# Kernel optimization log

Measured on AMD Instinct MI355X. Metric: run time of the kernel, lower is better.

The kernel has to match this reference:

```python
import jax, jax.numpy as jnp
import numpy as np

B, C, L = 8, 1024, 1024
H = 16
D = C // H  # 64 samples per head
GROUPS = 32  # GroupNorm32: channels > 64 -> 32 groups
EPS = 1e-5


def setup_inputs() -> dict:
    key = jax.random.key(0)
    ks = jax.random.split(key, 5)
    x = jax.random.normal(ks[0], (B, C, L), dtype=jnp.float32)
    gn_weight = jnp.ones((C,), jnp.float32)
    gn_bias = jnp.zeros((C,), jnp.float32)
    qkv_w = jax.random.normal(ks[1], (3 * C, C), jnp.float32) * 0.02
    qkv_b = jax.random.normal(ks[2], (3 * C,), jnp.float32) * 0.02
    out_w = jax.random.normal(ks[3], (C, C), jnp.float32) * 0.02
    out_b = jax.random.normal(ks[4], (C,), jnp.float32) * 0.02
    return {"x": x, "gn_weight": gn_weight, "gn_bias": gn_bias,
            "qkv_w": qkv_w, "qkv_b": qkv_b, "out_w": out_w, "out_b": out_b,
            "qk_bias": 0}


def _group_norm(x, w, b):
    # x: [B, C, L]; normalize over (C//GROUPS, L) per group, in float32
    xg = x.astype(jnp.float32).reshape(B, GROUPS, -1)
    mu = xg.mean(axis=-1, keepdims=True)
    var = xg.var(axis=-1, keepdims=True)
    xn = ((xg - mu) * jax.lax.rsqrt(var + EPS)).reshape(B, C, L)
    return (xn * w[None, :, None] + b[None, :, None]).astype(x.dtype)


def reference(x, gn_weight, gn_bias, qkv_w, qkv_b, out_w, out_b, qk_bias):
    scale = 1.0 / np.sqrt(D).astype(np.float32)
    xn = _group_norm(x, gn_weight, gn_bias)
    # 1x1 conv == pointwise matmul over channels
    qkv = jnp.einsum('oc,bcl->bol', qkv_w, xn) + qkv_b[None, :, None]  # [B,3C,L]
    # reshape (B, H, 3D, L) and split exactly as torch .split(D, dim=2)
    qkv = qkv.reshape(B, H, 3 * D, L)
    q, k, v = qkv[:, :, :D], qkv[:, :, D:2 * D], qkv[:, :, 2 * D:]
    q = jnp.swapaxes(q, -1, -2) * scale  # [B,H,L,D]
    k = k * scale                        # [B,H,D,L]
    v = jnp.swapaxes(v, -1, -2)          # [B,H,L,D]
    score = jnp.einsum('bhld,bhdm->bhlm', q, k) + qk_bias  # [B,H,L,L]
    weights = jax.nn.softmax(score.astype(jnp.float32), axis=-1)
    ctx = jnp.einsum('bhlm,bhmd->bhld', weights, v)  # [B,H,L,D]
    ctx = jnp.swapaxes(ctx, -1, -2).reshape(B, C, L)
    h = jnp.einsum('oc,bcl->bol', out_w, ctx) + out_b[None, :, None]
    return xn + h  # residual uses the normalized x, as in the source
```

## Files before the change

kernel.cpp:

```cpp
#include <hip/hip_runtime.h>

using bf16x8 = __attribute__((ext_vector_type(8))) __bf16;
using f32x4  = __attribute__((ext_vector_type(4))) float;
using f32x16 = __attribute__((ext_vector_type(16))) float;
typedef __attribute__((ext_vector_type(2))) unsigned u32x2;
typedef __attribute__((ext_vector_type(4))) unsigned u32x4;

#define DEV __device__ __forceinline__

DEV unsigned short f2bf(float f){
  unsigned u = __builtin_bit_cast(unsigned, f);
  u += 0x7fffu + ((u >> 16) & 1u);
  return (unsigned short)(u >> 16);
}

DEV void load_lds16(const void* g, void* l){
  __builtin_amdgcn_global_load_lds((const __attribute__((address_space(1))) unsigned*)g,
                                   (__attribute__((address_space(3))) unsigned*)l, 16, 0, 0);
}

DEV f32x4 mfma16(bf16x8 a, bf16x8 b, f32x4 c){
  return __builtin_amdgcn_mfma_f32_16x16x32_bf16(a, b, c, 0, 0, 0);
}

DEV f32x16 mfma32(bf16x8 a, bf16x8 b, f32x16 c){
  return __builtin_amdgcn_mfma_f32_32x32x16_bf16(a, b, c, 0, 0, 0);
}

DEV float exp2_hw(float x){
  float r;
  asm("v_exp_f32 %0, %1" : "=v"(r) : "v"(x));
  return r;
}

DEV unsigned cvtpk_bf16(float a, float b){
  unsigned r;
  asm("v_cvt_pk_bf16_f32 %0, %1, %2" : "=v"(r) : "v"(a), "v"(b));
  return r;
}

DEV void permswap(unsigned &a, unsigned &b){
  asm volatile("v_permlane32_swap_b32 %0, %1" : "+v"(a), "+v"(b));
}

__global__ void wconv_k(const float* __restrict__ a, unsigned short* __restrict__ o, int n4){
  for (int i = blockIdx.x * blockDim.x + threadIdx.x; i < n4; i += gridDim.x * blockDim.x){
    float4 v = reinterpret_cast<const float4*>(a)[i];
    ushort4 u;
    u.x = f2bf(v.x); u.y = f2bf(v.y); u.z = f2bf(v.z); u.w = f2bf(v.w);
    reinterpret_cast<ushort4*>(o)[i] = u;
  }
}

__global__ __launch_bounds__(256) void gn_stats_k(const float* __restrict__ x, float* __restrict__ st){
  int bg = blockIdx.x;
  const float4* xp = reinterpret_cast<const float4*>(x + (size_t)bg * 32768);
  float s = 0.f, ss = 0.f;
  for (int i = threadIdx.x; i < 8192; i += 256){
    float4 v = xp[i];
    s  += (v.x + v.y) + (v.z + v.w);
    ss += (v.x*v.x + v.y*v.y) + (v.z*v.z + v.w*v.w);
  }
  #pragma unroll
  for (int off = 32; off; off >>= 1){ s += __shfl_down(s, off); ss += __shfl_down(ss, off); }
  __shared__ float rs[4], rss[4];
  if ((threadIdx.x & 63) == 0){ rs[threadIdx.x >> 6] = s; rss[threadIdx.x >> 6] = ss; }
  __syncthreads();
  if (threadIdx.x == 0){
    s  = (rs[0] + rs[1]) + (rs[2] + rs[3]);
    ss = (rss[0] + rss[1]) + (rss[2] + rss[3]);
    float mu  = s * (1.0f / 32768.0f);
    float var = ss * (1.0f / 32768.0f) - mu * mu;
    st[bg*2]   = mu;
    st[bg*2+1] = rsqrtf(var + 1e-5f);
  }
}

__global__ __launch_bounds__(256) void gn_norm_k(const float* __restrict__ x,
                                                 const float* __restrict__ gw,
                                                 const float* __restrict__ gb,
                                                 const float* __restrict__ st,
                                                 float* __restrict__ xn,
                                                 unsigned short* __restrict__ xnt){
  int t = blockIdx.x;
  int tile = t & 15; int g = (t >> 4) & 31; int bb = t >> 9;
  float mu = st[(bb*32+g)*2], rstd = st[(bb*32+g)*2+1];
  __shared__ unsigned short lt[64*32];
  int tid = threadIdx.x;
  int l = tid & 63;
  int c0 = tid >> 6;
  size_t base = ((size_t)bb*1024 + g*32) * 1024 + tile*64;
  #pragma unroll
  for (int cb = 0; cb < 8; ++cb){
    int c = cb*4 + c0;
    size_t idx = base + (size_t)c*1024 + l;
    float xv = x[idx];
    int cg = g*32 + c;
    float v = (xv - mu) * rstd * gw[cg] + gb[cg];
    xn[idx] = v;
    lt[l*32 + c] = f2bf(v);
  }
  __syncthreads();
  int lr = tid >> 2, sl = tid & 3;
  uint4 u = *reinterpret_cast<uint4*>(&lt[lr*32 + sl*8]);
  size_t ob = ((size_t)bb*1024 + tile*64 + lr) * 1024 + g*32 + sl*8;
  *reinterpret_cast<uint4*>(&xnt[ob]) = u;
}

template<int MODE>
__global__ __launch_bounds__(256) void gemm_k(const unsigned short* __restrict__ A,
                                              const unsigned short* __restrict__ Bm,
                                              const float* __restrict__ bias,
                                              float* __restrict__ outf,
                                              unsigned short* __restrict__ qo,
                                              unsigned short* __restrict__ ko,
                                              unsigned short* __restrict__ vo){
  constexpr int MT = MODE ? 8 : 24;
  constexpr int CHUNK = MT * 8;
  __shared__ char sA[16384];
  __shared__ char sB[16384];
  const int tid = threadIdx.x;
  const int w = tid >> 6, ln = tid & 63, hi = ln >> 4, lo = ln & 15;
  const int wrow = w >> 1, wcol = w & 1;
  const int bxo = (int)blockIdx.x;
  const int bx = (bxo & 7) * CHUNK + (bxo >> 3);
  const int b = bx / (MT*8);
  const int rem = bx % (MT*8);
  const int mt = rem >> 3, nt = rem & 7;
  const char* Ag = (const char*)A + (size_t)mt*128*2048;
  const char* Bg = (const char*)Bm + ((size_t)b*1024 + nt*128)*2048;
  f32x4 acc[4][4] = {};
  for (int kk = 0; kk < 16; ++kk){
    #pragma unroll
    for (int i = 0; i < 4; ++i){
      int s = tid*16 + i*4096;
      int row = s >> 7;
      int byte = (s & 127) ^ ((row & 7) << 4);
      size_t off = (size_t)row*2048 + kk*128 + byte;
      load_lds16(Ag + off, sA + s);
      load_lds16(Bg + off, sB + s);
    }
    __syncthreads();
    #pragma unroll
    for (int ks = 0; ks < 2; ++ks){
      bf16x8 af[4], bq[4];
      #pragma unroll
      for (int mi = 0; mi < 4; ++mi){
        int row = wrow*64 + mi*16 + lo;
        af[mi] = *reinterpret_cast<const bf16x8*>(sA + row*128 + ((ks*64 + hi*16) ^ ((row & 7) << 4)));
      }
      #pragma unroll
      for (int ni = 0; ni < 4; ++ni){
        int row = wcol*64 + ni*16 + lo;
        bq[ni] = *reinterpret_cast<const bf16x8*>(sB + row*128 + ((ks*64 + hi*16) ^ ((row & 7) << 4)));
      }
      #pragma unroll
      for (int mi = 0; mi < 4; ++mi)
        #pragma unroll
        for (int ni = 0; ni < 4; ++ni)
          acc[mi][ni] = mfma16(af[mi], bq[ni], acc[mi][ni]);
    }
    __syncthreads();
  }
  if (MODE == 0){
    #pragma unroll
    for (int mi = 0; mi < 4; ++mi){
      const int o0 = mt*128 + wrow*64 + mi*16 + hi*4;
      const int hh = o0 / 192;
      const int rr = o0 % 192;
      const size_t hb = (size_t)b*16 + hh;
      float bv0 = bias[o0], bv1 = bias[o0+1], bv2 = bias[o0+2], bv3 = bias[o0+3];
      #pragma unroll
      for (int ni = 0; ni < 4; ++ni){
        const int l = nt*128 + wcol*64 + ni*16 + lo;
        if (rr < 64){
          ushort4 u;
          u.x = f2bf(acc[mi][ni][0] + bv0); u.y = f2bf(acc[mi][ni][1] + bv1);
          u.z = f2bf(acc[mi][ni][2] + bv2); u.w = f2bf(acc[mi][ni][3] + bv3);
          *reinterpret_cast<ushort4*>(qo + (hb*1024 + l)*64 + rr) = u;
        } else if (rr < 128){
          ushort4 u;
          u.x = f2bf(acc[mi][ni][0] + bv0); u.y = f2bf(acc[mi][ni][1] + bv1);
          u.z = f2bf(acc[mi][ni][2] + bv2); u.w = f2bf(acc[mi][ni][3] + bv3);
          *reinterpret_cast<ushort4*>(ko + (hb*1024 + l)*64 + (rr - 64)) = u;
        } else {
          const int d = rr - 128;
          vo[(hb*64 + d + 0)*1024 + l] = f2bf(acc[mi][ni][0] + bv0);
          vo[(hb*64 + d + 1)*1024 + l] = f2bf(acc[mi][ni][1] + bv1);
          vo[(hb*64 + d + 2)*1024 + l] = f2bf(acc[mi][ni][2] + bv2);
          vo[(hb*64 + d + 3)*1024 + l] = f2bf(acc[mi][ni][3] + bv3);
        }
      }
    }
  } else {
    #pragma unroll
    for (int mi = 0; mi < 4; ++mi){
      const int o0 = mt*128 + wrow*64 + mi*16 + hi*4;
      #pragma unroll
      for (int ni = 0; ni < 4; ++ni){
        const int l = nt*128 + wcol*64 + ni*16 + lo;
        #pragma unroll
        for (int r = 0; r < 4; ++r){
          size_t idx = ((size_t)b*1024 + o0 + r) * 1024 + l;
          outf[idx] += acc[mi][ni][r] + bias[o0 + r];
        }
      }
    }
  }
}

__global__ __launch_bounds__(256) void attn_k(const unsigned short* __restrict__ qt,
                                              const unsigned short* __restrict__ kt,
                                              const unsigned short* __restrict__ vt,
                                              unsigned short* __restrict__ ctx){
  __shared__ char sK[2][8192];
  __shared__ char sV[2][8192];
  __shared__ float sRed[4][32];
  const int tid = threadIdx.x;
  const int w = tid >> 6, ln = tid & 63;
  const int hi5 = ln >> 5, lo5 = ln & 31;
  const int bxo = (int)blockIdx.x;
  const int bx = (bxo & 7) * 128 + (bxo >> 3);
  const int qb = bx & 7;
  const int bh = bx >> 3;
  const unsigned short* qp = qt + ((size_t)bh*1024 + qb*128 + w*32 + lo5) * 64;
  bf16x8 qreg[4];
  #pragma unroll
  for (int d = 0; d < 4; ++d)
    qreg[d] = *reinterpret_cast<const bf16x8*>(qp + d*16 + hi5*8);
  const char* kg = (const char*)(kt + (size_t)bh*65536);
  const char* vg = (const char*)(vt + (size_t)bh*65536);
  f32x16 oa0 = {}, oa1 = {};
  float m = 0.f, l = 0.f;

  auto STAGE = [&](int buf, int kb){
    #pragma unroll
    for (int i = 0; i < 2; ++i){
      int s = tid*16 + i*4096;
      int row = s >> 7;
      int byte = (s & 127) ^ ((row & 7) << 4);
      load_lds16(kg + (size_t)(kb*64 + row)*128 + byte, sK[buf] + s);
      load_lds16(vg + (size_t)row*2048 + kb*128 + byte, sV[buf] + s);
    }
  };

  const float sc2 = 0.015625f * 1.44269504f;

  STAGE(0, 0);
  asm volatile("s_waitcnt vmcnt(0)" ::: "memory");
  __builtin_amdgcn_s_barrier();

  for (int kb = 0; kb < 16; ++kb){
    const int cur = kb & 1;
    STAGE(cur ^ 1, (kb + 1) & 15);

    const char* kbase0 = sK[cur] + lo5*128;
    const char* kbase1 = sK[cur] + (32 + lo5)*128;
    const int ksw = (lo5 & 7) << 4;
    f32x16 s0 = {}, s1 = {};
    #pragma unroll
    for (int d = 0; d < 4; ++d){
      int off = (d*32 + hi5*16) ^ ksw;
      bf16x8 ka = *reinterpret_cast<const bf16x8*>(kbase0 + off);
      bf16x8 kb8 = *reinterpret_cast<const bf16x8*>(kbase1 + off);
      s0 = mfma32(ka, qreg[d], s0);
      s1 = mfma32(kb8, qreg[d], s1);
    }

    float t[16];
    #pragma unroll
    for (int i = 0; i < 16; ++i) t[i] = fmaxf(s0[i], s1[i]);
    #pragma unroll
    for (int st = 8; st; st >>= 1)
      #pragma unroll
      for (int i = 0; i < st; ++i) t[i] = fmaxf(t[i], t[i+st]);
    float mx = fmaxf(t[0], __shfl_xor(t[0], 32));
    float m2 = mx * sc2;

    if (__builtin_expect(__any(m2 > m + 8.f), 0)){
      float nm = fmaxf(m, m2);
      float corr = exp2_hw(m - nm);
      m = nm; l *= corr;
      sRed[w][lo5] = corr;
      __builtin_amdgcn_wave_barrier();
      #pragma unroll
      for (int r = 0; r < 16; ++r){
        float cc = sRed[w][(r & 3) + 8*(r >> 2) + 4*hi5];
        oa0[r] *= cc; oa1[r] *= cc;
      }
      __builtin_amdgcn_wave_barrier();
    }

    float ps[16];
    #pragma unroll
    for (int i = 0; i < 16; ++i){
      float p0 = exp2_hw(fmaf(s0[i], sc2, -m));
      float p1 = exp2_hw(fmaf(s1[i], sc2, -m));
      s0[i] = p0; s1[i] = p1;
      ps[i] = p0 + p1;
    }
    #pragma unroll
    for (int st = 8; st; st >>= 1)
      #pragma unroll
      for (int i = 0; i < st; ++i) ps[i] += ps[i+st];
    l += ps[0] + __shfl_xor(ps[0], 32);

    bf16x8 pa[4];
    #pragma unroll
    for (int sl = 0; sl < 4; ++sl){
      const int c0 = 2*(sl & 1), c1 = c0 + 1;
      unsigned w0, w1, w2, w3;
      if (sl < 2){
        w0 = cvtpk_bf16(s0[4*c0+0], s0[4*c0+1]);
        w1 = cvtpk_bf16(s0[4*c0+2], s0[4*c0+3]);
        w2 = cvtpk_bf16(s0[4*c1+0], s0[4*c1+1]);
        w3 = cvtpk_bf16(s0[4*c1+2], s0[4*c1+3]);
      } else {
        w0 = cvtpk_bf16(s1[4*c0+0], s1[4*c0+1]);
        w1 = cvtpk_bf16(s1[4*c0+2], s1[4*c0+3]);
        w2 = cvtpk_bf16(s1[4*c1+0], s1[4*c1+1]);
        w3 = cvtpk_bf16(s1[4*c1+2], s1[4*c1+3]);
      }
      permswap(w0, w2);
      permswap(w1, w3);
      u32x4 pc; pc.x = w0; pc.y = w1; pc.z = w2; pc.w = w3;
      pa[sl] = __builtin_bit_cast(bf16x8, pc);
    }

    const char* vb0 = sV[cur] + lo5*128;
    const char* vb1 = sV[cur] + (32 + lo5)*128;
    #pragma unroll
    for (int sl = 0; sl < 4; ++sl){
      int off = (sl*32 + hi5*16) ^ ksw;
      bf16x8 v0 = *reinterpret_cast<const bf16x8*>(vb0 + off);
      bf16x8 v1 = *reinterpret_cast<const bf16x8*>(vb1 + off);
      oa0 = mfma32(pa[sl], v0, oa0);
      oa1 = mfma32(pa[sl], v1, oa1);
    }

    asm volatile("s_waitcnt vmcnt(0)" ::: "memory");
    __builtin_amdgcn_s_barrier();
  }

  sRed[w][lo5] = l;
  __builtin_amdgcn_wave_barrier();
  const int b = bh >> 4, h = bh & 15;
  #pragma unroll
  for (int r = 0; r < 16; ++r){
    int ql = (r & 3) + 8*(r >> 2) + 4*hi5;
    float inv = __builtin_amdgcn_rcpf(sRed[w][ql]);
    size_t rowb = ((size_t)b*1024 + qb*128 + w*32 + ql) * 1024 + h*64;
    ctx[rowb + lo5]      = f2bf(oa0[r] * inv);
    ctx[rowb + 32 + lo5] = f2bf(oa1[r] * inv);
  }
}

extern "C" void kernel_launch(void* const* d_in, const int* in_sizes, int n_in,
                              void* d_out, int out_size, void* d_ws, size_t ws_size,
                              hipStream_t stream) {
  (void)in_sizes; (void)n_in; (void)out_size; (void)ws_size;
  const float* x     = (const float*)d_in[0];
  const float* gn_w  = (const float*)d_in[1];
  const float* gn_b  = (const float*)d_in[2];
  const float* qkv_w = (const float*)d_in[3];
  const float* qkv_b = (const float*)d_in[4];
  const float* out_w = (const float*)d_in[5];
  const float* out_b = (const float*)d_in[6];
  float* out = (float*)d_out;
  char* ws = (char*)d_ws;
  unsigned short* xnt  = (unsigned short*)(ws);
  unsigned short* qwb  = (unsigned short*)(ws + 16777216);
  unsigned short* owb  = (unsigned short*)(ws + 23068672);
  unsigned short* qt   = (unsigned short*)(ws + 25165824);
  unsigned short* kt   = (unsigned short*)(ws + 41943040);
  unsigned short* vs   = (unsigned short*)(ws + 58720256);
  unsigned short* ctxt = (unsigned short*)(ws + 75497472);
  float*          st   = (float*)(ws + 92274688);

  wconv_k<<<512, 256, 0, stream>>>(qkv_w, qwb, 786432);
  wconv_k<<<512, 256, 0, stream>>>(out_w, owb, 262144);
  gn_stats_k<<<256, 256, 0, stream>>>(x, st);
  gn_norm_k<<<4096, 256, 0, stream>>>(x, gn_w, gn_b, st, out, xnt);
  gemm_k<0><<<1536, 256, 0, stream>>>(qwb, xnt, qkv_b, nullptr, qt, kt, vs);
  attn_k<<<1024, 256, 0, stream>>>(qt, kt, vs, ctxt);
  gemm_k<1><<<512, 256, 0, stream>>>(owb, ctxt, out_b, out, nullptr, nullptr, nullptr);
}
```

Measured before the change: 288.1 us.

## Replace QKV GEMM with 256x256 tile, 8-wave, double-buffered pipelined kernel

```diff
diff --git a/kernel.cpp b/kernel.cpp
--- a/kernel.cpp
+++ b/kernel.cpp
@@ -107,15 +107,178 @@
   *reinterpret_cast<uint4*>(&xnt[ob]) = u;
 }
 
-template<int MODE>
+__global__ __launch_bounds__(512, 2) void gemm8_k(const unsigned short* __restrict__ A,
+                                                  const unsigned short* __restrict__ Bm,
+                                                  const float* __restrict__ bias,
+                                                  unsigned short* __restrict__ qo,
+                                                  unsigned short* __restrict__ ko,
+                                                  unsigned short* __restrict__ vo){
+  __shared__ char sA[2][32768];
+  __shared__ char sB[2][32768];
+  const int tid = threadIdx.x;
+  const int w = tid >> 6, ln = tid & 63, hi = ln >> 4, lo = ln & 15;
+  const int wm = w >> 2, wn = w & 3;
+  const int bxo = (int)blockIdx.x;
+  const int bx = (bxo & 7) * 48 + (bxo >> 3);
+  const int mt = bx >> 5, nt = bx & 31;
+  const char* Ag = (const char*)A + (size_t)mt*256*2048;
+  const char* Bg = (const char*)Bm + (size_t)nt*256*2048;
+  f32x4 acc[8][4] = {};
+
+  auto stageA = [&](int buf, int kk, int i){
+    int s = tid*16 + i*8192;
+    int row = s >> 7;
+    int byte = (s & 127) ^ ((row & 7) << 4);
+    load_lds16(Ag + (size_t)row*2048 + kk*128 + byte, sA[buf] + s);
+  };
+  auto stageB = [&](int buf, int kk, int i){
+    int s = tid*16 + i*8192;
+    int row = s >> 7;
+    int byte = (s & 127) ^ ((row & 7) << 4);
+    load_lds16(Bg + (size_t)row*2048 + kk*128 + byte, sB[buf] + s);
+  };
+
+  #pragma unroll
+  for (int i = 0; i < 4; ++i){ stageA(0, 0, i); stageB(0, 0, i); }
+  asm volatile("s_waitcnt vmcnt(0)" ::: "memory");
+  __builtin_amdgcn_s_barrier();
+
+  for (int t = 0; t < 16; ++t){
+    const int cur = t & 1;
+    const int nxt = cur ^ 1;
+    const int k2 = (t + 1) & 15;
+    const bool st = (t < 15);
+    const char* sAc = sA[cur];
+    const char* sBc = sB[cur];
+    bf16x8 a[4][2], b[2][2];
+
+    #pragma unroll
+    for (int mi = 0; mi < 4; ++mi){
+      int row = wm*128 + mi*16 + lo;
+      #pragma unroll
+      for (int ks = 0; ks < 2; ++ks)
+        a[mi][ks] = *reinterpret_cast<const bf16x8*>(sAc + row*128 + ((ks*64 + hi*16) ^ ((row & 7) << 4)));
+    }
+    #pragma unroll
+    for (int ni = 0; ni < 2; ++ni){
+      int row = wn*64 + ni*16 + lo;
+      #pragma unroll
+      for (int ks = 0; ks < 2; ++ks)
+        b[ni][ks] = *reinterpret_cast<const bf16x8*>(sBc + row*128 + ((ks*64 + hi*16) ^ ((row & 7) << 4)));
+    }
+    if (st){ stageA(nxt, k2, 0); stageA(nxt, k2, 1); }
+    __builtin_amdgcn_s_barrier();
+    __builtin_amdgcn_s_setprio(1);
+    #pragma unroll
+    for (int mi = 0; mi < 4; ++mi)
+      #pragma unroll
+      for (int ni = 0; ni < 2; ++ni)
+        #pragma unroll
+        for (int ks = 0; ks < 2; ++ks)
+          acc[mi][ni] = mfma16(a[mi][ks], b[ni][ks], acc[mi][ni]);
+    __builtin_amdgcn_s_setprio(0);
+    __builtin_amdgcn_s_barrier();
+
+    #pragma unroll
+    for (int ni = 0; ni < 2; ++ni){
+      int row = wn*64 + 32 + ni*16 + lo;
+      #pragma unroll
+      for (int ks = 0; ks < 2; ++ks)
+        b[ni][ks] = *reinterpret_cast<const bf16x8*>(sBc + row*128 + ((ks*64 + hi*16) ^ ((row & 7) << 4)));
+    }
+    if (st){ stageA(nxt, k2, 2); stageA(nxt, k2, 3); }
+    __builtin_amdgcn_s_barrier();
+    __builtin_amdgcn_s_setprio(1);
+    #pragma unroll
+    for (int mi = 0; mi < 4; ++mi)
+      #pragma unroll
+      for (int ni = 0; ni < 2; ++ni)
+        #pragma unroll
+        for (int ks = 0; ks < 2; ++ks)
+          acc[mi][2+ni] = mfma16(a[mi][ks], b[ni][ks], acc[mi][2+ni]);
+    __builtin_amdgcn_s_setprio(0);
+    __builtin_amdgcn_s_barrier();
+
+    #pragma unroll
+    for (int mi = 0; mi < 4; ++mi){
+      int row = wm*128 + 64 + mi*16 + lo;
+      #pragma unroll
+      for (int ks = 0; ks < 2; ++ks)
+        a[mi][ks] = *reinterpret_cast<const bf16x8*>(sAc + row*128 + ((ks*64 + hi*16) ^ ((row & 7) << 4)));
+    }
+    if (st){ stageB(nxt, k2, 0); stageB(nxt, k2, 1); }
+    __builtin_amdgcn_s_barrier();
+    __builtin_amdgcn_s_setprio(1);
+    #pragma unroll
+    for (int mi = 0; mi < 4; ++mi)
+      #pragma unroll
+      for (int ni = 0; ni < 2; ++ni)
+        #pragma unroll
+        for (int ks = 0; ks < 2; ++ks)
+          acc[4+mi][2+ni] = mfma16(a[mi][ks], b[ni][ks], acc[4+mi][2+ni]);
+    __builtin_amdgcn_s_setprio(0);
+    __builtin_amdgcn_s_barrier();
+
+    #pragma unroll
+    for (int ni = 0; ni < 2; ++ni){
+      int row = wn*64 + ni*16 + lo;
+      #pragma unroll
+      for (int ks = 0; ks < 2; ++ks)
+        b[ni][ks] = *reinterpret_cast<const bf16x8*>(sBc + row*128 + ((ks*64 + hi*16) ^ ((row & 7) << 4)));
+    }
+    if (st){ stageB(nxt, k2, 2); stageB(nxt, k2, 3); }
+    __builtin_amdgcn_s_barrier();
+    __builtin_amdgcn_s_setprio(1);
+    #pragma unroll
+    for (int mi = 0; mi < 4; ++mi)
+      #pragma unroll
+      for (int ni = 0; ni < 2; ++ni)
+        #pragma unroll
+        for (int ks = 0; ks < 2; ++ks)
+          acc[4+mi][ni] = mfma16(a[mi][ks], b[ni][ks], acc[4+mi][ni]);
+    __builtin_amdgcn_s_setprio(0);
+    asm volatile("s_waitcnt vmcnt(0)" ::: "memory");
+    __builtin_amdgcn_s_barrier();
+  }
+
+  const int b = nt >> 2;
+  #pragma unroll
+  for (int m8 = 0; m8 < 8; ++m8){
+    const int o0 = mt*256 + wm*128 + (m8 >> 2)*64 + (m8 & 3)*16 + hi*4;
+    const int hh = o0 / 192;
+    const int rr = o0 % 192;
+    const size_t hb = (size_t)b*16 + hh;
+    float bv0 = bias[o0], bv1 = bias[o0+1], bv2 = bias[o0+2], bv3 = bias[o0+3];
+    #pragma unroll
+    for (int n4 = 0; n4 < 4; ++n4){
+      const int l = (nt & 3)*256 + wn*64 + (n4 >> 1)*32 + (n4 & 1)*16 + lo;
+      f32x4 v = acc[m8][n4];
+      if (rr < 64){
+        ushort4 u;
+        u.x = f2bf(v[0] + bv0); u.y = f2bf(v[1] + bv1);
+        u.z = f2bf(v[2] + bv2); u.w = f2bf(v[3] + bv3);
+        *reinterpret_cast<ushort4*>(qo + (hb*1024 + l)*64 + rr) = u;
+      } else if (rr < 128){
+        ushort4 u;
+        u.x = f2bf(v[0] + bv0); u.y = f2bf(v[1] + bv1);
+        u.z = f2bf(v[2] + bv2); u.w = f2bf(v[3] + bv3);
+        *reinterpret_cast<ushort4*>(ko + (hb*1024 + l)*64 + (rr - 64)) = u;
+      } else {
+        const int d = rr - 128;
+        vo[(hb*64 + d + 0)*1024 + l] = f2bf(v[0] + bv0);
+        vo[(hb*64 + d + 1)*1024 + l] = f2bf(v[1] + bv1);
+        vo[(hb*64 + d + 2)*1024 + l] = f2bf(v[2] + bv2);
+        vo[(hb*64 + d + 3)*1024 + l] = f2bf(v[3] + bv3);
+      }
+    }
+  }
+}
+
 __global__ __launch_bounds__(256) void gemm_k(const unsigned short* __restrict__ A,
                                               const unsigned short* __restrict__ Bm,
                                               const float* __restrict__ bias,
-                                              float* __restrict__ outf,
-                                              unsigned short* __restrict__ qo,
-                                              unsigned short* __restrict__ ko,
-                                              unsigned short* __restrict__ vo){
-  constexpr int MT = MODE ? 8 : 24;
+                                              float* __restrict__ outf){
+  constexpr int MT = 8;
   constexpr int CHUNK = MT * 8;
   __shared__ char sA[16384];
   __shared__ char sB[16384];
@@ -162,48 +325,16 @@
     }
     __syncthreads();
   }
-  if (MODE == 0){
-    #pragma unroll
-    for (int mi = 0; mi < 4; ++mi){
-      const int o0 = mt*128 + wrow*64 + mi*16 + hi*4;
-      const int hh = o0 / 192;
-      const int rr = o0 % 192;
-      const size_t hb = (size_t)b*16 + hh;
-      float bv0 = bias[o0], bv1 = bias[o0+1], bv2 = bias[o0+2], bv3 = bias[o0+3];
-      #pragma unroll
-      for (int ni = 0; ni < 4; ++ni){
-        const int l = nt*128 + wcol*64 + ni*16 + lo;
-        if (rr < 64){
-          ushort4 u;
-          u.x = f2bf(acc[mi][ni][0] + bv0); u.y = f2bf(acc[mi][ni][1] + bv1);
-          u.z = f2bf(acc[mi][ni][2] + bv2); u.w = f2bf(acc[mi][ni][3] + bv3);
-          *reinterpret_cast<ushort4*>(qo + (hb*1024 + l)*64 + rr) = u;
-        } else if (rr < 128){
-          ushort4 u;
-          u.x = f2bf(acc[mi][ni][0] + bv0); u.y = f2bf(acc[mi][ni][1] + bv1);
-          u.z = f2bf(acc[mi][ni][2] + bv2); u.w = f2bf(acc[mi][ni][3] + bv3);
-          *reinterpret_cast<ushort4*>(ko + (hb*1024 + l)*64 + (rr - 64)) = u;
-        } else {
-          const int d = rr - 128;
-          vo[(hb*64 + d + 0)*1024 + l] = f2bf(acc[mi][ni][0] + bv0);
-          vo[(hb*64 + d + 1)*1024 + l] = f2bf(acc[mi][ni][1] + bv1);
-          vo[(hb*64 + d + 2)*1024 + l] = f2bf(acc[mi][ni][2] + bv2);
-          vo[(hb*64 + d + 3)*1024 + l] = f2bf(acc[mi][ni][3] + bv3);
-        }
-      }
-    }
-  } else {
-    #pragma unroll
-    for (int mi = 0; mi < 4; ++mi){
-      const int o0 = mt*128 + wrow*64 + mi*16 + hi*4;
-      #pragma unroll
-      for (int ni = 0; ni < 4; ++ni){
-        const int l = nt*128 + wcol*64 + ni*16 + lo;
-        #pragma unroll
-        for (int r = 0; r < 4; ++r){
-          size_t idx = ((size_t)b*1024 + o0 + r) * 1024 + l;
-          outf[idx] += acc[mi][ni][r] + bias[o0 + r];
-        }
+  #pragma unroll
+  for (int mi = 0; mi < 4; ++mi){
+    const int o0 = mt*128 + wrow*64 + mi*16 + hi*4;
+    #pragma unroll
+    for (int ni = 0; ni < 4; ++ni){
+      const int l = nt*128 + wcol*64 + ni*16 + lo;
+      #pragma unroll
+      for (int r = 0; r < 4; ++r){
+        size_t idx = ((size_t)b*1024 + o0 + r) * 1024 + l;
+        outf[idx] += acc[mi][ni][r] + bias[o0 + r];
       }
     }
   }
@@ -381,7 +512,7 @@
   wconv_k<<<512, 256, 0, stream>>>(out_w, owb, 262144);
   gn_stats_k<<<256, 256, 0, stream>>>(x, st);
   gn_norm_k<<<4096, 256, 0, stream>>>(x, gn_w, gn_b, st, out, xnt);
-  gemm_k<0><<<1536, 256, 0, stream>>>(qwb, xnt, qkv_b, nullptr, qt, kt, vs);
+  gemm8_k<<<384, 512, 0, stream>>>(qwb, xnt, qkv_b, qt, kt, vs);
   attn_k<<<1024, 256, 0, stream>>>(qt, kt, vs, ctxt);
-  gemm_k<1><<<512, 256, 0, stream>>>(owb, ctxt, out_b, out, nullptr, nullptr, nullptr);
-}
+  gemm_k<<<512, 256, 0, stream>>>(owb, ctxt, out_b, out);
+}
```

After: 302.9 us. 5.1% more time.

## Replace QKV GEMM with 256x256-tile, 8-wave double-buffered pipelined kernel

Applied to the files above, without the earlier changes.

```diff
diff --git a/kernel.cpp b/kernel.cpp
--- a/kernel.cpp
+++ b/kernel.cpp
@@ -107,15 +107,164 @@
   *reinterpret_cast<uint4*>(&xnt[ob]) = u;
 }
 
-template<int MODE>
+__global__ __launch_bounds__(512, 2) void gemm8_k(const unsigned short* __restrict__ A,
+                                                  const unsigned short* __restrict__ Bm,
+                                                  const float* __restrict__ bias,
+                                                  unsigned short* __restrict__ qo,
+                                                  unsigned short* __restrict__ ko,
+                                                  unsigned short* __restrict__ vo){
+  __shared__ char sA[2][32768];
+  __shared__ char sB[2][32768];
+  const int tid = threadIdx.x;
+  const int w = tid >> 6, ln = tid & 63, hi = ln >> 4, lo = ln & 15;
+  const int wm = w >> 2, wn = w & 3;
+  const int bxo = (int)blockIdx.x;
+  const int xcd = bxo & 7, idx = bxo >> 3;
+  const int mt = (xcd >> 2)*6 + (idx % 6);
+  const int nt = (xcd & 3)*8 + (idx / 6);
+  const char* Ag = (const char*)A + (size_t)mt*256*2048;
+  const char* Bg = (const char*)Bm + (size_t)nt*256*2048;
+  f32x4 acc[8][4] = {};
+
+  auto stageA = [&](int buf, int kt, int kh, int mh){
+    const int lr = tid >> 2;
+    const int cslot = (tid & 3) ^ ((lr >> 1) & 3);
+    const int r = mh*64 + (lr & 63) + ((lr & 64) << 1);
+    load_lds16(Ag + (size_t)r*2048 + kt*128 + kh*64 + cslot*16,
+               sA[buf] + (kh*2 + mh)*8192 + tid*16);
+  };
+  auto stageB = [&](int buf, int kt, int kh, int i){
+    const int s = tid*16 + i*8192;
+    const int r = s >> 6;
+    const int cslot = ((s >> 4) & 3) ^ ((r >> 1) & 3);
+    load_lds16(Bg + (size_t)r*2048 + kt*128 + kh*64 + cslot*16,
+               sB[buf] + kh*16384 + s);
+  };
+  auto readA = [&](const char* base, int kh, int mh, int mi){
+    const int lr = wm*64 + mi*16 + lo;
+    return *reinterpret_cast<const bf16x8*>(base + (kh*2 + mh)*8192 + lr*64 + ((hi ^ ((lr >> 1) & 3)) << 4));
+  };
+  auto readB = [&](const char* base, int kh, int ni){
+    const int r = wn*64 + ni*16 + lo;
+    return *reinterpret_cast<const bf16x8*>(base + kh*16384 + r*64 + ((hi ^ ((r >> 1) & 3)) << 4));
+  };
+
+  stageB(0, 0, 0, 0); stageB(0, 0, 0, 1);
+  stageA(0, 0, 0, 0); stageA(0, 0, 0, 1);
+  stageB(0, 0, 1, 0); stageB(0, 0, 1, 1);
+  stageA(0, 0, 1, 0); stageA(0, 0, 1, 1);
+
+  bf16x8 a[4], b[4];
+  #define MFMA_CLUSTER(AOFF)                                        \
+    __builtin_amdgcn_s_setprio(1);                                  \
+    _Pragma("unroll")                                               \
+    for (int mi = 0; mi < 4; ++mi)                                  \
+      _Pragma("unroll")                                             \
+      for (int ni = 0; ni < 4; ++ni)                                \
+        acc[AOFF + mi][ni] = mfma16(a[mi], b[ni], acc[AOFF + mi][ni]); \
+    __builtin_amdgcn_s_setprio(0);
+
+  for (int t = 0; t < 15; ++t){
+    const int cur = t & 1, nxt = cur ^ 1, tn = t + 1;
+    const char* sAc = sA[cur];
+    const char* sBc = sB[cur];
+    asm volatile("s_waitcnt vmcnt(5)" ::: "memory");
+    __builtin_amdgcn_s_barrier();
+    stageB(nxt, tn, 0, 0); stageB(nxt, tn, 0, 1);
+    #pragma unroll
+    for (int ni = 0; ni < 4; ++ni) b[ni] = readB(sBc, 0, ni);
+    #pragma unroll
+    for (int mi = 0; mi < 4; ++mi) a[mi] = readA(sAc, 0, 0, mi);
+    MFMA_CLUSTER(0)
+    asm volatile("s_waitcnt vmcnt(6)" ::: "memory");
+    __builtin_amdgcn_s_barrier();
+    stageA(nxt, tn, 0, 0); stageA(nxt, tn, 0, 1);
+    #pragma unroll
+    for (int mi = 0; mi < 4; ++mi) a[mi] = readA(sAc, 0, 1, mi);
+    MFMA_CLUSTER(4)
+    asm volatile("s_waitcnt vmcnt(5)" ::: "memory");
+    __builtin_amdgcn_s_barrier();
+    stageB(nxt, tn, 1, 0); stageB(nxt, tn, 1, 1);
+    #pragma unroll
+    for (int ni = 0; ni < 4; ++ni) b[ni] = readB(sBc, 1, ni);
+    #pragma unroll
+    for (int mi = 0; mi < 4; ++mi) a[mi] = readA(sAc, 1, 0, mi);
+    MFMA_CLUSTER(0)
+    asm volatile("s_waitcnt vmcnt(6)" ::: "memory");
+    __builtin_amdgcn_s_barrier();
+    stageA(nxt, tn, 1, 0); stageA(nxt, tn, 1, 1);
+    #pragma unroll
+    for (int mi = 0; mi < 4; ++mi) a[mi] = readA(sAc, 1, 1, mi);
+    MFMA_CLUSTER(4)
+  }
+  {
+    const char* sAc = sA[1];
+    const char* sBc = sB[1];
+    asm volatile("s_waitcnt vmcnt(5)" ::: "memory");
+    __builtin_amdgcn_s_barrier();
+    #pragma unroll
+    for (int ni = 0; ni < 4; ++ni) b[ni] = readB(sBc, 0, ni);
+    #pragma unroll
+    for (int mi = 0; mi < 4; ++mi) a[mi] = readA(sAc, 0, 0, mi);
+    MFMA_CLUSTER(0)
+    asm volatile("s_waitcnt vmcnt(4)" ::: "memory");
+    __builtin_amdgcn_s_barrier();
+    #pragma unroll
+    for (int mi = 0; mi < 4; ++mi) a[mi] = readA(sAc, 0, 1, mi);
+    MFMA_CLUSTER(4)
+    asm volatile("s_waitcnt vmcnt(1)" ::: "memory");
+    __builtin_amdgcn_s_barrier();
+    #pragma unroll
+    for (int ni = 0; ni < 4; ++ni) b[ni] = readB(sBc, 1, ni);
+    #pragma unroll
+    for (int mi = 0; mi < 4; ++mi) a[mi] = readA(sAc, 1, 0, mi);
+    MFMA_CLUSTER(0)
+    asm volatile("s_waitcnt vmcnt(0)" ::: "memory");
+    __builtin_amdgcn_s_barrier();
+    #pragma unroll
+    for (int mi = 0; mi < 4; ++mi) a[mi] = readA(sAc, 1, 1, mi);
+    MFMA_CLUSTER(4)
+  }
+  #undef MFMA_CLUSTER
+
+  const int b8 = nt >> 2;
+  #pragma unroll
+  for (int m8 = 0; m8 < 8; ++m8){
+    const int o0 = mt*256 + wm*128 + (m8 >> 2)*64 + (m8 & 3)*16 + hi*4;
+    const int hh = o0 / 192;
+    const int rr = o0 % 192;
+    const size_t hb = (size_t)b8*16 + hh;
+    float bv0 = bias[o0], bv1 = bias[o0+1], bv2 = bias[o0+2], bv3 = bias[o0+3];
+    #pragma unroll
+    for (int n4 = 0; n4 < 4; ++n4){
+      const int l = (nt & 3)*256 + wn*64 + (n4 >> 1)*32 + (n4 & 1)*16 + lo;
+      f32x4 v = acc[m8][n4];
+      if (rr < 64){
+        ushort4 u;
+        u.x = f2bf(v[0] + bv0); u.y = f2bf(v[1] + bv1);
+        u.z = f2bf(v[2] + bv2); u.w = f2bf(v[3] + bv3);
+        *reinterpret_cast<ushort4*>(qo + (hb*1024 + l)*64 + rr) = u;
+      } else if (rr < 128){
+        ushort4 u;
+        u.x = f2bf(v[0] + bv0); u.y = f2bf(v[1] + bv1);
+        u.z = f2bf(v[2] + bv2); u.w = f2bf(v[3] + bv3);
+        *reinterpret_cast<ushort4*>(ko + (hb*1024 + l)*64 + (rr - 64)) = u;
+      } else {
+        const int d = rr - 128;
+        vo[(hb*64 + d + 0)*1024 + l] = f2bf(v[0] + bv0);
+        vo[(hb*64 + d + 1)*1024 + l] = f2bf(v[1] + bv1);
+        vo[(hb*64 + d + 2)*1024 + l] = f2bf(v[2] + bv2);
+        vo[(hb*64 + d + 3)*1024 + l] = f2bf(v[3] + bv3);
+      }
+    }
+  }
+}
+
 __global__ __launch_bounds__(256) void gemm_k(const unsigned short* __restrict__ A,
                                               const unsigned short* __restrict__ Bm,
                                               const float* __restrict__ bias,
-                                              float* __restrict__ outf,
-                                              unsigned short* __restrict__ qo,
-                                              unsigned short* __restrict__ ko,
-                                              unsigned short* __restrict__ vo){
-  constexpr int MT = MODE ? 8 : 24;
+                                              float* __restrict__ outf){
+  constexpr int MT = 8;
   constexpr int CHUNK = MT * 8;
   __shared__ char sA[16384];
   __shared__ char sB[16384];
@@ -162,48 +311,16 @@
     }
     __syncthreads();
   }
-  if (MODE == 0){
-    #pragma unroll
-    for (int mi = 0; mi < 4; ++mi){
-      const int o0 = mt*128 + wrow*64 + mi*16 + hi*4;
-      const int hh = o0 / 192;
-      const int rr = o0 % 192;
-      const size_t hb = (size_t)b*16 + hh;
-      float bv0 = bias[o0], bv1 = bias[o0+1], bv2 = bias[o0+2], bv3 = bias[o0+3];
-      #pragma unroll
-      for (int ni = 0; ni < 4; ++ni){
-        const int l = nt*128 + wcol*64 + ni*16 + lo;
-        if (rr < 64){
-          ushort4 u;
-          u.x = f2bf(acc[mi][ni][0] + bv0); u.y = f2bf(acc[mi][ni][1] + bv1);
-          u.z = f2bf(acc[mi][ni][2] + bv2); u.w = f2bf(acc[mi][ni][3] + bv3);
-          *reinterpret_cast<ushort4*>(qo + (hb*1024 + l)*64 + rr) = u;
-        } else if (rr < 128){
-          ushort4 u;
-          u.x = f2bf(acc[mi][ni][0] + bv0); u.y = f2bf(acc[mi][ni][1] + bv1);
-          u.z = f2bf(acc[mi][ni][2] + bv2); u.w = f2bf(acc[mi][ni][3] + bv3);
-          *reinterpret_cast<ushort4*>(ko + (hb*1024 + l)*64 + (rr - 64)) = u;
-        } else {
-          const int d = rr - 128;
-          vo[(hb*64 + d + 0)*1024 + l] = f2bf(acc[mi][ni][0] + bv0);
-          vo[(hb*64 + d + 1)*1024 + l] = f2bf(acc[mi][ni][1] + bv1);
-          vo[(hb*64 + d + 2)*1024 + l] = f2bf(acc[mi][ni][2] + bv2);
-          vo[(hb*64 + d + 3)*1024 + l] = f2bf(acc[mi][ni][3] + bv3);
-        }
-      }
-    }
-  } else {
-    #pragma unroll
-    for (int mi = 0; mi < 4; ++mi){
-      const int o0 = mt*128 + wrow*64 + mi*16 + hi*4;
-      #pragma unroll
-      for (int ni = 0; ni < 4; ++ni){
-        const int l = nt*128 + wcol*64 + ni*16 + lo;
-        #pragma unroll
-        for (int r = 0; r < 4; ++r){
-          size_t idx = ((size_t)b*1024 + o0 + r) * 1024 + l;
-          outf[idx] += acc[mi][ni][r] + bias[o0 + r];
-        }
+  #pragma unroll
+  for (int mi = 0; mi < 4; ++mi){
+    const int o0 = mt*128 + wrow*64 + mi*16 + hi*4;
+    #pragma unroll
+    for (int ni = 0; ni < 4; ++ni){
+      const int l = nt*128 + wcol*64 + ni*16 + lo;
+      #pragma unroll
+      for (int r = 0; r < 4; ++r){
+        size_t idx = ((size_t)b*1024 + o0 + r) * 1024 + l;
+        outf[idx] += acc[mi][ni][r] + bias[o0 + r];
       }
     }
   }
@@ -381,7 +498,7 @@
   wconv_k<<<512, 256, 0, stream>>>(out_w, owb, 262144);
   gn_stats_k<<<256, 256, 0, stream>>>(x, st);
   gn_norm_k<<<4096, 256, 0, stream>>>(x, gn_w, gn_b, st, out, xnt);
-  gemm_k<0><<<1536, 256, 0, stream>>>(qwb, xnt, qkv_b, nullptr, qt, kt, vs);
+  gemm8_k<<<384, 512, 0, stream>>>(qwb, xnt, qkv_b, qt, kt, vs);
   attn_k<<<1024, 256, 0, stream>>>(qt, kt, vs, ctxt);
-  gemm_k<1><<<512, 256, 0, stream>>>(owb, ctxt, out_b, out, nullptr, nullptr, nullptr);
-}
+  gemm_k<<<512, 256, 0, stream>>>(owb, ctxt, out_b, out);
+}
```

After: 309.9 us. 1.08x slower.

## Double-buffer GEMM LDS staging with 128x256 tiles and XCD-aware block mapping

Applied to the files above, without the earlier changes.

```diff
diff --git a/kernel.cpp b/kernel.cpp
--- a/kernel.cpp
+++ b/kernel.cpp
@@ -108,101 +108,141 @@
 }
 
 template<int MODE>
-__global__ __launch_bounds__(256) void gemm_k(const unsigned short* __restrict__ A,
-                                              const unsigned short* __restrict__ Bm,
-                                              const float* __restrict__ bias,
-                                              float* __restrict__ outf,
-                                              unsigned short* __restrict__ qo,
-                                              unsigned short* __restrict__ ko,
-                                              unsigned short* __restrict__ vo){
-  constexpr int MT = MODE ? 8 : 24;
-  constexpr int CHUNK = MT * 8;
-  __shared__ char sA[16384];
-  __shared__ char sB[16384];
+__global__ __launch_bounds__(512, 2) void gemmT_k(const unsigned short* __restrict__ A,
+                                                  const unsigned short* __restrict__ Bm,
+                                                  const float* __restrict__ bias,
+                                                  float* __restrict__ outf,
+                                                  unsigned short* __restrict__ qo,
+                                                  unsigned short* __restrict__ ko,
+                                                  unsigned short* __restrict__ vo){
+  __shared__ char sA[2][16384];
+  __shared__ char sB[2][32768];
   const int tid = threadIdx.x;
   const int w = tid >> 6, ln = tid & 63, hi = ln >> 4, lo = ln & 15;
-  const int wrow = w >> 1, wcol = w & 1;
+  const int wm = w >> 2, wn = w & 3;
   const int bxo = (int)blockIdx.x;
-  const int bx = (bxo & 7) * CHUNK + (bxo >> 3);
-  const int b = bx / (MT*8);
-  const int rem = bx % (MT*8);
-  const int mt = rem >> 3, nt = rem & 7;
+  constexpr int MH = (MODE == 0 ? 12 : 4);
+  const int xcd = bxo & 7, idx = bxo >> 3;
+  const int mt = (xcd >> 2)*MH + idx % MH;
+  const int nt = (xcd & 3)*8 + idx / MH;
   const char* Ag = (const char*)A + (size_t)mt*128*2048;
-  const char* Bg = (const char*)Bm + ((size_t)b*1024 + nt*128)*2048;
+  const char* Bg = (const char*)Bm + (size_t)nt*256*2048;
   f32x4 acc[4][4] = {};
-  for (int kk = 0; kk < 16; ++kk){
-    #pragma unroll
-    for (int i = 0; i < 4; ++i){
-      int s = tid*16 + i*4096;
-      int row = s >> 7;
-      int byte = (s & 127) ^ ((row & 7) << 4);
-      size_t off = (size_t)row*2048 + kk*128 + byte;
-      load_lds16(Ag + off, sA + s);
-      load_lds16(Bg + off, sB + s);
-    }
-    __syncthreads();
-    #pragma unroll
-    for (int ks = 0; ks < 2; ++ks){
-      bf16x8 af[4], bq[4];
-      #pragma unroll
-      for (int mi = 0; mi < 4; ++mi){
-        int row = wrow*64 + mi*16 + lo;
-        af[mi] = *reinterpret_cast<const bf16x8*>(sA + row*128 + ((ks*64 + hi*16) ^ ((row & 7) << 4)));
-      }
-      #pragma unroll
-      for (int ni = 0; ni < 4; ++ni){
-        int row = wcol*64 + ni*16 + lo;
-        bq[ni] = *reinterpret_cast<const bf16x8*>(sB + row*128 + ((ks*64 + hi*16) ^ ((row & 7) << 4)));
-      }
-      #pragma unroll
-      for (int mi = 0; mi < 4; ++mi)
-        #pragma unroll
-        for (int ni = 0; ni < 4; ++ni)
-          acc[mi][ni] = mfma16(af[mi], bq[ni], acc[mi][ni]);
-    }
-    __syncthreads();
-  }
+
+  auto stageA = [&](int buf, int kt, int i){
+    int s = tid*16 + i*8192;
+    int row = s >> 7;
+    int byte = (s & 127) ^ ((row & 7) << 4);
+    load_lds16(Ag + (size_t)row*2048 + kt*128 + byte, sA[buf] + s);
+  };
+  auto stageB = [&](int buf, int kt, int i){
+    int s = tid*16 + i*8192;
+    int row = s >> 7;
+    int byte = (s & 127) ^ ((row & 7) << 4);
+    load_lds16(Bg + (size_t)row*2048 + kt*128 + byte, sB[buf] + s);
+  };
+
+  stageB(0,0,0); stageB(0,0,1); stageB(0,0,2); stageB(0,0,3);
+  stageA(0,0,0); stageA(0,0,1);
+  asm volatile("s_waitcnt vmcnt(0)" ::: "memory");
+  __builtin_amdgcn_s_barrier();
+
+  for (int t = 0; t < 16; ++t){
+    const int cur = t & 1, nxt = cur ^ 1;
+    const bool st = (t < 15);
+    const char* sAc = sA[cur];
+    const char* sBc = sB[cur];
+    bf16x8 a[4], b[4];
+
+    #pragma unroll
+    for (int mi = 0; mi < 4; ++mi){
+      int row = wm*64 + mi*16 + lo;
+      a[mi] = *reinterpret_cast<const bf16x8*>(sAc + row*128 + ((hi*16) ^ ((row & 7) << 4)));
+    }
+    #pragma unroll
+    for (int ni = 0; ni < 4; ++ni){
+      int row = wn*64 + ni*16 + lo;
+      b[ni] = *reinterpret_cast<const bf16x8*>(sBc + row*128 + ((hi*16) ^ ((row & 7) << 4)));
+    }
+    if (st){
+      stageB(nxt,t+1,0); stageB(nxt,t+1,1); stageB(nxt,t+1,2); stageB(nxt,t+1,3);
+      stageA(nxt,t+1,0); stageA(nxt,t+1,1);
+    }
+    __builtin_amdgcn_s_barrier();
+    __builtin_amdgcn_s_setprio(1);
+    #pragma unroll
+    for (int mi = 0; mi < 4; ++mi)
+      #pragma unroll
+      for (int ni = 0; ni < 4; ++ni)
+        acc[mi][ni] = mfma16(a[mi], b[ni], acc[mi][ni]);
+    __builtin_amdgcn_s_setprio(0);
+    __builtin_amdgcn_s_barrier();
+
+    #pragma unroll
+    for (int mi = 0; mi < 4; ++mi){
+      int row = wm*64 + mi*16 + lo;
+      a[mi] = *reinterpret_cast<const bf16x8*>(sAc + row*128 + ((64 + hi*16) ^ ((row & 7) << 4)));
+    }
+    #pragma unroll
+    for (int ni = 0; ni < 4; ++ni){
+      int row = wn*64 + ni*16 + lo;
+      b[ni] = *reinterpret_cast<const bf16x8*>(sBc + row*128 + ((64 + hi*16) ^ ((row & 7) << 4)));
+    }
+    __builtin_amdgcn_s_barrier();
+    __builtin_amdgcn_s_setprio(1);
+    #pragma unroll
+    for (int mi = 0; mi < 4; ++mi)
+      #pragma unroll
+      for (int ni = 0; ni < 4; ++ni)
+        acc[mi][ni] = mfma16(a[mi], b[ni], acc[mi][ni]);
+    __builtin_amdgcn_s_setprio(0);
+    if (st) asm volatile("s_waitcnt vmcnt(0)" ::: "memory");
+    __builtin_amdgcn_s_barrier();
+  }
+
+  const int b8 = nt >> 2;
   if (MODE == 0){
     #pragma unroll
     for (int mi = 0; mi < 4; ++mi){
-      const int o0 = mt*128 + wrow*64 + mi*16 + hi*4;
+      const int o0 = mt*128 + wm*64 + mi*16 + hi*4;
       const int hh = o0 / 192;
       const int rr = o0 % 192;
-      const size_t hb = (size_t)b*16 + hh;
+      const size_t hb = (size_t)b8*16 + hh;
       float bv0 = bias[o0], bv1 = bias[o0+1], bv2 = bias[o0+2], bv3 = bias[o0+3];
       #pragma unroll
       for (int ni = 0; ni < 4; ++ni){
-        const int l = nt*128 + wcol*64 + ni*16 + lo;
+        const int l = (nt & 3)*256 + wn*64 + ni*16 + lo;
+        f32x4 v = acc[mi][ni];
         if (rr < 64){
           ushort4 u;
-          u.x = f2bf(acc[mi][ni][0] + bv0); u.y = f2bf(acc[mi][ni][1] + bv1);
-          u.z = f2bf(acc[mi][ni][2] + bv2); u.w = f2bf(acc[mi][ni][3] + bv3);
+          u.x = f2bf(v[0] + bv0); u.y = f2bf(v[1] + bv1);
+          u.z = f2bf(v[2] + bv2); u.w = f2bf(v[3] + bv3);
           *reinterpret_cast<ushort4*>(qo + (hb*1024 + l)*64 + rr) = u;
         } else if (rr < 128){
           ushort4 u;
-          u.x = f2bf(acc[mi][ni][0] + bv0); u.y = f2bf(acc[mi][ni][1] + bv1);
-          u.z = f2bf(acc[mi][ni][2] + bv2); u.w = f2bf(acc[mi][ni][3] + bv3);
+          u.x = f2bf(v[0] + bv0); u.y = f2bf(v[1] + bv1);
+          u.z = f2bf(v[2] + bv2); u.w = f2bf(v[3] + bv3);
           *reinterpret_cast<ushort4*>(ko + (hb*1024 + l)*64 + (rr - 64)) = u;
         } else {
           const int d = rr - 128;
-          vo[(hb*64 + d + 0)*1024 + l] = f2bf(acc[mi][ni][0] + bv0);
-          vo[(hb*64 + d + 1)*1024 + l] = f2bf(acc[mi][ni][1] + bv1);
-          vo[(hb*64 + d + 2)*1024 + l] = f2bf(acc[mi][ni][2] + bv2);
-          vo[(hb*64 + d + 3)*1024 + l] = f2bf(acc[mi][ni][3] + bv3);
+          vo[(hb*64 + d + 0)*1024 + l] = f2bf(v[0] + bv0);
+          vo[(hb*64 + d + 1)*1024 + l] = f2bf(v[1] + bv1);
+          vo[(hb*64 + d + 2)*1024 + l] = f2bf(v[2] + bv2);
+          vo[(hb*64 + d + 3)*1024 + l] = f2bf(v[3] + bv3);
         }
       }
     }
   } else {
     #pragma unroll
     for (int mi = 0; mi < 4; ++mi){
-      const int o0 = mt*128 + wrow*64 + mi*16 + hi*4;
+      const int o0 = mt*128 + wm*64 + mi*16 + hi*4;
       #pragma unroll
       for (int ni = 0; ni < 4; ++ni){
-        const int l = nt*128 + wcol*64 + ni*16 + lo;
+        const int l = (nt & 3)*256 + wn*64 + ni*16 + lo;
         #pragma unroll
         for (int r = 0; r < 4; ++r){
-          size_t idx = ((size_t)b*1024 + o0 + r) * 1024 + l;
-          outf[idx] += acc[mi][ni][r] + bias[o0 + r];
+          size_t idx2 = ((size_t)b8*1024 + o0 + r) * 1024 + l;
+          outf[idx2] += acc[mi][ni][r] + bias[o0 + r];
         }
       }
     }
@@ -381,7 +421,7 @@
   wconv_k<<<512, 256, 0, stream>>>(out_w, owb, 262144);
   gn_stats_k<<<256, 256, 0, stream>>>(x, st);
   gn_norm_k<<<4096, 256, 0, stream>>>(x, gn_w, gn_b, st, out, xnt);
-  gemm_k<0><<<1536, 256, 0, stream>>>(qwb, xnt, qkv_b, nullptr, qt, kt, vs);
+  gemmT_k<0><<<768, 512, 0, stream>>>(qwb, xnt, qkv_b, nullptr, qt, kt, vs);
   attn_k<<<1024, 256, 0, stream>>>(qt, kt, vs, ctxt);
-  gemm_k<1><<<512, 256, 0, stream>>>(owb, ctxt, out_b, out, nullptr, nullptr, nullptr);
-}
+  gemmT_k<1><<<256, 512, 0, stream>>>(owb, ctxt, out_b, out, nullptr, nullptr, nullptr);
+}
```

Measured after the change: 292.6 us. No clear change (+1.6%).
